# Kernel tuning notes

Measured on AMD Instinct MI355X. Metric: run time of the kernel, lower is better.

## Reference

```python
import jax, jax.numpy as jnp
import numpy as np

H = 512   # lstm_hidden_size
B = 64    # batch
S = 256   # seqlen


def setup_inputs() -> dict:
    key = jax.random.key(0)
    ks = jax.random.split(key, 6)
    scale = 1.0 / np.sqrt(H)  # PyTorch LSTM default init range
    return {
        "x": jax.random.normal(ks[0], (B, S, 2 * H), dtype=jnp.float32),
        "hi": jax.random.normal(ks[1], (B, S, 2 * H), dtype=jnp.float32),
        "W_ih": jax.random.uniform(ks[2], (4 * H, 5 * H), minval=-scale, maxval=scale, dtype=jnp.float32),
        "W_hh": jax.random.uniform(ks[3], (4 * H, H), minval=-scale, maxval=scale, dtype=jnp.float32),
        "b_ih": jax.random.uniform(ks[4], (4 * H,), minval=-scale, maxval=scale, dtype=jnp.float32),
        "b_hh": jax.random.uniform(ks[5], (4 * H,), minval=-scale, maxval=scale, dtype=jnp.float32),
    }


def _forward(x, hi, W_ih, W_hh, b_ih, b_hh):
    h_dim = W_hh.shape[1]
    bias = b_ih + b_hh
    xc = jnp.concatenate([x, hi], axis=-1)          # [B, S, 4H]
    xc = jnp.transpose(xc, (1, 0, 2))               # [S, B, 4H]
    batch = xc.shape[1]

    def cell(hc, inp_b):
        # inp_b: [5H]; PyTorch LSTM treats the batch dim as seq (batch_first=False quirk)
        h, c = hc
        gates = inp_b @ W_ih.T + h @ W_hh.T + bias  # [4H]
        i_g, f_g, g_g, o_g = jnp.split(gates, 4)
        i_g = jax.nn.sigmoid(i_g)
        f_g = jax.nn.sigmoid(f_g)
        g_g = jnp.tanh(g_g)
        o_g = jax.nn.sigmoid(o_g)
        c = f_g * c + i_g * g_g
        h = o_g * jnp.tanh(c)
        return (h, c), h

    def step(carry, x_i):
        out_prev, h, c = carry                      # out_prev: [B, H]
        inp = jnp.concatenate([x_i, out_prev], axis=-1)  # [B, 5H]
        (h, c), outs = jax.lax.scan(cell, (h, c), inp)    # scan over batch dim
        return (outs, h, c), outs

    init = (jnp.zeros((batch, h_dim), x.dtype),
            jnp.zeros((h_dim,), x.dtype),
            jnp.zeros((h_dim,), x.dtype))
    _, all_out = jax.lax.scan(step, init, xc)       # [S, B, H]
    return jnp.transpose(all_out, (1, 0, 2))        # [B, S, H]


def reference(x, hi, W_ih, W_hh, b_ih, b_hh):
    # Dropout layers are identity in eval mode.
    return _forward(x, hi, W_ih, W_hh, b_ih, b_hh)
```

## Files before the change

kernel.cpp:

```cpp
#include <hip/hip_runtime.h>

typedef _Float16 f16;
typedef _Float16 f16x2 __attribute__((ext_vector_type(2)));
typedef _Float16 f16x4 __attribute__((ext_vector_type(4)));
typedef _Float16 f16x8 __attribute__((ext_vector_type(8)));
typedef float f32x4 __attribute__((ext_vector_type(4)));
typedef unsigned int u32;
typedef unsigned int u32x4 __attribute__((ext_vector_type(4)));
typedef unsigned long long ull;

#define HD 512
#define T_TOT 16384
#define RING 128
#define NWG 32
#define NTH 512

static const size_t O_XC    = 0;
static const size_t O_W1    = 67108864;
static const size_t O_WHH   = 75497472;
static const size_t O_W2    = 77594624;
static const size_t O_G     = 79691776;
static const size_t O_PRING = 213909504;

__device__ __forceinline__ float dot2f(f16x2 a, f16x2 b, float c) {
#if __has_builtin(__builtin_amdgcn_fdot2)
    return __builtin_amdgcn_fdot2(a, b, c, false);
#else
    return fmaf((float)a[0], (float)b[0], fmaf((float)a[1], (float)b[1], c));
#endif
}
__device__ __forceinline__ f16x2 bcf(u32 u) { return __builtin_bit_cast(f16x2, u); }

__device__ __forceinline__ float sigf(float x) { return 1.0f / (1.0f + __expf(-x)); }
__device__ __forceinline__ float tanhfast(float x) { return 1.0f - 2.0f / (__expf(2.0f * x) + 1.0f); }

__device__ __forceinline__ ull ld_a64(const ull* p) {
    return __hip_atomic_load(p, __ATOMIC_RELAXED, __HIP_MEMORY_SCOPE_AGENT);
}
__device__ __forceinline__ void st_a64(ull* p, ull v) {
    __hip_atomic_store(p, v, __ATOMIC_RELAXED, __HIP_MEMORY_SCOPE_AGENT);
}

__global__ __launch_bounds__(256) void conv_xc(const float* __restrict__ x,
                                               const float* __restrict__ hi,
                                               f16* __restrict__ xc) {
    int gid = blockIdx.x * 256 + threadIdx.x;
    int t = gid >> 9;
    int k = (gid & 511) << 2;
    int b = t & 63, s = t >> 6;
    const float* src = (k < 1024) ? (x  + ((size_t)((b << 8) + s) << 10) + k)
                                  : (hi + ((size_t)((b << 8) + s) << 10) + (k - 1024));
    float4 v = *reinterpret_cast<const float4*>(src);
    f16x4 o = { (_Float16)v.x, (_Float16)v.y, (_Float16)v.z, (_Float16)v.w };
    *reinterpret_cast<f16x4*>(xc + ((size_t)t << 11) + k) = o;
}

__global__ __launch_bounds__(256) void conv_w1(const float* __restrict__ wih,
                                               f16* __restrict__ w1) {
    int gid = blockIdx.x * 256 + threadIdx.x;
    int j = gid >> 9;
    int k = (gid & 511) << 2;
    float4 v = *reinterpret_cast<const float4*>(wih + (size_t)j * 2560 + k);
    f16x4 o = { (_Float16)v.x, (_Float16)v.y, (_Float16)v.z, (_Float16)v.w };
    *reinterpret_cast<f16x4*>(w1 + ((size_t)j << 11) + k) = o;
}

__global__ __launch_bounds__(256) void conv_wc(const float* __restrict__ whh,
                                               const float* __restrict__ wih,
                                               f16* __restrict__ whhf,
                                               f16* __restrict__ w2f) {
    int gid = blockIdx.x * 256 + threadIdx.x;
    int j = gid >> 7;
    int k = (gid & 127) << 2;
    float4 a = *reinterpret_cast<const float4*>(whh + (size_t)j * 512 + k);
    f16x4 oa = { (_Float16)a.x, (_Float16)a.y, (_Float16)a.z, (_Float16)a.w };
    *reinterpret_cast<f16x4*>(whhf + ((size_t)j << 9) + k) = oa;
    float4 bv = *reinterpret_cast<const float4*>(wih + (size_t)j * 2560 + 2048 + k);
    f16x4 ob = { (_Float16)bv.x, (_Float16)bv.y, (_Float16)bv.z, (_Float16)bv.w };
    *reinterpret_cast<f16x4*>(w2f + ((size_t)j << 9) + k) = ob;
}

__global__ __launch_bounds__(256) void gemm_pre(const f16* __restrict__ XC,
                                                const f16* __restrict__ W1,
                                                const float* __restrict__ b_ih,
                                                const float* __restrict__ b_hh,
                                                float* __restrict__ G) {
    int w = threadIdx.x >> 6, l = threadIdx.x & 63;
    int R0 = blockIdx.y * 128 + (w >> 1) * 64;
    int C0 = blockIdx.x * 128 + (w & 1) * 64;
    int lr = l & 15, kb = l >> 4;
    f32x4 acc[4][4] = {};
    const f16* Abase = XC + (size_t)(R0 + lr) * 2048 + kb * 8;
    const f16* Bbase = W1 + (size_t)(C0 + lr) * 2048 + kb * 8;
    for (int kk = 0; kk < 2048; kk += 32) {
        f16x8 av[4], bv[4];
#pragma unroll
        for (int i = 0; i < 4; i++)
            av[i] = *reinterpret_cast<const f16x8*>(Abase + (size_t)(i * 16) * 2048 + kk);
#pragma unroll
        for (int i = 0; i < 4; i++)
            bv[i] = *reinterpret_cast<const f16x8*>(Bbase + (size_t)(i * 16) * 2048 + kk);
#pragma unroll
        for (int fr = 0; fr < 4; fr++)
#pragma unroll
            for (int fc = 0; fc < 4; fc++)
                acc[fr][fc] = __builtin_amdgcn_mfma_f32_16x16x32_f16(av[fr], bv[fc], acc[fr][fc], 0, 0, 0);
    }
#pragma unroll
    for (int fc = 0; fc < 4; fc++) {
        int col = C0 + fc * 16 + lr;
        float bias = b_ih[col] + b_hh[col];
#pragma unroll
        for (int fr = 0; fr < 4; fr++) {
#pragma unroll
            for (int r = 0; r < 4; r++) {
                int row = R0 + fr * 16 + kb * 4 + r;
                G[(size_t)row * 2048 + col] = acc[fr][fc][r] + bias;
            }
        }
    }
}

__global__ __launch_bounds__(NTH, 1) void lstm_chain(const float* __restrict__ G,
                                                     const f16* __restrict__ Whhf,
                                                     const f16* __restrict__ W2f,
                                                     ull* __restrict__ ring,
                                                     float* __restrict__ out) {
    const int wg = blockIdx.x;
    const int tid = threadIdx.x;
    const int wv = tid >> 6, l = tid & 63;
    const int g = wv & 3, uh = wv >> 2;
    const int rr = ((l & 1) << 2) | (l & 2) | ((l >> 2) & 1);
    const int row0 = g * 512 + wg * 16 + uh * 8;
    const int growD = row0 + rr;

    __shared__ u32 hist[64][256];
    __shared__ __align__(16) float part[2][16][4];

    for (int i = tid; i < 4096; i += NTH)
        reinterpret_cast<u32x4*>(hist)[i] = (u32x4){0u, 0u, 0u, 0u};

    u32 wu1[32], wu2[32];
#pragma unroll
    for (int r = 0; r < 8; r++) {
        u32x4 a = __builtin_bit_cast(u32x4,
            *reinterpret_cast<const f16x8*>(Whhf + (size_t)(row0 + r) * 512 + 8 * l));
        u32x4 b = __builtin_bit_cast(u32x4,
            *reinterpret_cast<const f16x8*>(W2f + (size_t)(row0 + r) * 512 + 8 * l));
        wu1[r * 4 + 0] = a.x; wu1[r * 4 + 1] = a.y; wu1[r * 4 + 2] = a.z; wu1[r * 4 + 3] = a.w;
        wu2[r * 4 + 0] = b.x; wu2[r * 4 + 1] = b.y; wu2[r * 4 + 2] = b.z; wu2[r * 4 + 3] = b.w;
    }
#pragma unroll
    for (int i = 0; i < 32; i++)
        asm volatile("" : "+v"(wu1[i]), "+v"(wu2[i]));

    float cst = 0.0f;
    float gv = (l < 8) ? G[growD] : 0.0f;
    __syncthreads();

    for (int t = 0; t < T_TOT; t++) {
        const int buf = t & 1;

        u32x4 hv = *reinterpret_cast<const u32x4*>(&hist[t & 63][4 * l]);
        float ac[8] = {0.f, 0.f, 0.f, 0.f, 0.f, 0.f, 0.f, 0.f};
        {
            f16x2 h0 = bcf(hv.x), h1 = bcf(hv.y), h2 = bcf(hv.z), h3 = bcf(hv.w);
#pragma unroll
            for (int r = 0; r < 8; r++) {
                ac[r] = dot2f(bcf(wu2[r * 4 + 0]), h0, ac[r]);
                ac[r] = dot2f(bcf(wu2[r * 4 + 1]), h1, ac[r]);
                ac[r] = dot2f(bcf(wu2[r * 4 + 2]), h2, ac[r]);
                ac[r] = dot2f(bcf(wu2[r * 4 + 3]), h3, ac[r]);
            }
        }

        const ull* pB = ring + (size_t)((t - 1) & (RING - 1)) * 256 + 4 * l;
        const u32 want = (u32)t;
        ull b0 = ld_a64(pB + 0), b1 = ld_a64(pB + 1);
        ull b2 = ld_a64(pB + 2), b3 = ld_a64(pB + 3);
        while ((((u32)(b0 >> 32) ^ want) | ((u32)(b1 >> 32) ^ want) |
                ((u32)(b2 >> 32) ^ want) | ((u32)(b3 >> 32) ^ want)) != 0u) {
            b0 = ld_a64(pB + 0); b1 = ld_a64(pB + 1);
            b2 = ld_a64(pB + 2); b3 = ld_a64(pB + 3);
        }

        int tn = (t + 1 < T_TOT) ? t + 1 : t;
        float gnext = (l < 8) ? G[(size_t)tn * 2048 + growD] : 0.0f;

        if (wv == 0)
            *reinterpret_cast<u32x4*>(&hist[(t - 1) & 63][4 * l]) =
                (u32x4){(u32)b0, (u32)b1, (u32)b2, (u32)b3};

        {
            f16x2 h0 = bcf((u32)b0), h1 = bcf((u32)b1), h2 = bcf((u32)b2), h3 = bcf((u32)b3);
#pragma unroll
            for (int r = 0; r < 8; r++) {
                ac[r] = dot2f(bcf(wu1[r * 4 + 0]), h0, ac[r]);
                ac[r] = dot2f(bcf(wu1[r * 4 + 1]), h1, ac[r]);
                ac[r] = dot2f(bcf(wu1[r * 4 + 2]), h2, ac[r]);
                ac[r] = dot2f(bcf(wu1[r * 4 + 3]), h3, ac[r]);
            }
        }

        const bool s0 = l & 1, s1 = l & 2, s2 = l & 4;
        float b4_0 = (s0 ? ac[4] : ac[0]) + __shfl_xor((s0 ? ac[0] : ac[4]), 1);
        float b4_1 = (s0 ? ac[5] : ac[1]) + __shfl_xor((s0 ? ac[1] : ac[5]), 1);
        float b4_2 = (s0 ? ac[6] : ac[2]) + __shfl_xor((s0 ? ac[2] : ac[6]), 1);
        float b4_3 = (s0 ? ac[7] : ac[3]) + __shfl_xor((s0 ? ac[3] : ac[7]), 1);
        float c2_0 = (s1 ? b4_2 : b4_0) + __shfl_xor((s1 ? b4_0 : b4_2), 2);
        float c2_1 = (s1 ? b4_3 : b4_1) + __shfl_xor((s1 ? b4_1 : b4_3), 2);
        float d    = (s2 ? c2_1 : c2_0) + __shfl_xor((s2 ? c2_0 : c2_1), 4);
        d += __shfl_xor(d, 8);
        d += __shfl_xor(d, 16);
        d += __shfl_xor(d, 32);
        if (l < 8)
            part[buf][uh * 8 + rr][g] = d + gv;
        gv = gnext;
        __syncthreads();

        const int u = l & 15;
        float4 pg = *reinterpret_cast<const float4*>(part[buf][u]);
        float fi = sigf(pg.x), ff = sigf(pg.y);
        float fgg = tanhfast(pg.z), fo = sigf(pg.w);
        cst = ff * cst + fi * fgg;
        float h = fo * tanhfast(cst);

        u32 hb = (u32)__builtin_bit_cast(unsigned short, (f16)h);
        u32 plo = (u32)__shfl((int)hb, 2 * (l & 7));
        u32 phi = (u32)__shfl((int)hb, 2 * (l & 7) + 1);
        ull pv = (ull)(plo & 0xffffu) | ((ull)(phi & 0xffffu) << 16) |
                 ((ull)(u32)(t + 1) << 32);
        if (wv == 0 && l < 8)
            st_a64(ring + (size_t)(t & (RING - 1)) * 256 + wg * 8 + l, pv);
        if (wv == 1 && l < 16) {
            int b = t & 63, s = t >> 6;
            out[((size_t)((b << 8) + s)) * 512 + wg * 16 + l] = h;
        }
    }
}

extern "C" void kernel_launch(void* const* d_in, const int* in_sizes, int n_in,
                              void* d_out, int out_size, void* d_ws, size_t ws_size,
                              hipStream_t stream) {
    const float* x    = (const float*)d_in[0];
    const float* hi   = (const float*)d_in[1];
    const float* W_ih = (const float*)d_in[2];
    const float* W_hh = (const float*)d_in[3];
    const float* b_ih = (const float*)d_in[4];
    const float* b_hh = (const float*)d_in[5];

    char* ws = (char*)d_ws;
    f16*   XCf   = (f16*)(ws + O_XC);
    f16*   W1f   = (f16*)(ws + O_W1);
    f16*   Whhf  = (f16*)(ws + O_WHH);
    f16*   W2f   = (f16*)(ws + O_W2);
    float* G     = (float*)(ws + O_G);
    ull*   ring  = (ull*)(ws + O_PRING);

    hipMemsetAsync(ring, 0, (size_t)RING * 256 * sizeof(ull), stream);

    conv_xc<<<32768, 256, 0, stream>>>(x, hi, XCf);
    conv_w1<<<4096, 256, 0, stream>>>(W_ih, W1f);
    conv_wc<<<1024, 256, 0, stream>>>(W_hh, W_ih, Whhf, W2f);
    gemm_pre<<<dim3(16, 128), 256, 0, stream>>>(XCf, W1f, b_ih, b_hh, G);
    lstm_chain<<<NWG, NTH, 0, stream>>>(G, Whhf, W2f, ring, (float*)d_out);
}
```

Measured before the change: 30.51 ms.

## Restructure LSTM chain to 64 single-wave blocks without LDS or barriers

The recurrent chain kernel moves from 32 workgroups of 8 waves to 64 single-wave workgroups. Each wave holds 32 rows of both recurrent weight matrices in registers, loaded with inline-asm vector loads. The intra-block shared-memory partial-sum exchange and __syncthreads per step are replaced by a wider shuffle reduction. The local LDS history buffer is dropped and the delayed h is reread from the global ring (slot t+64). This removes per-step barrier and LDS latency from the serial critical path, at the cost of very high register pressure per lane, more global ring traffic, and double the number of inter-block flag polls.

```diff
diff --git a/kernel.cpp b/kernel.cpp
--- a/kernel.cpp
+++ b/kernel.cpp
@@ -12,8 +12,7 @@
 #define HD 512
 #define T_TOT 16384
 #define RING 128
-#define NWG 32
-#define NTH 512
+#define NWAVE 64
 
 static const size_t O_XC    = 0;
 static const size_t O_W1    = 67108864;
@@ -121,60 +120,86 @@
     }
 }
 
-__global__ __launch_bounds__(NTH, 1) void lstm_chain(const float* __restrict__ G,
-                                                     const f16* __restrict__ Whhf,
-                                                     const f16* __restrict__ W2f,
-                                                     ull* __restrict__ ring,
-                                                     float* __restrict__ out) {
-    const int wg = blockIdx.x;
-    const int tid = threadIdx.x;
-    const int wv = tid >> 6, l = tid & 63;
-    const int g = wv & 3, uh = wv >> 2;
-    const int rr = ((l & 1) << 2) | (l & 2) | ((l >> 2) & 1);
-    const int row0 = g * 512 + wg * 16 + uh * 8;
-    const int growD = row0 + rr;
-
-    __shared__ u32 hist[64][256];
-    __shared__ __align__(16) float part[2][16][4];
-
-    for (int i = tid; i < 4096; i += NTH)
-        reinterpret_cast<u32x4*>(hist)[i] = (u32x4){0u, 0u, 0u, 0u};
-
-    u32 wu1[32], wu2[32];
-#pragma unroll
-    for (int r = 0; r < 8; r++) {
-        u32x4 a = __builtin_bit_cast(u32x4,
-            *reinterpret_cast<const f16x8*>(Whhf + (size_t)(row0 + r) * 512 + 8 * l));
-        u32x4 b = __builtin_bit_cast(u32x4,
-            *reinterpret_cast<const f16x8*>(W2f + (size_t)(row0 + r) * 512 + 8 * l));
-        wu1[r * 4 + 0] = a.x; wu1[r * 4 + 1] = a.y; wu1[r * 4 + 2] = a.z; wu1[r * 4 + 3] = a.w;
-        wu2[r * 4 + 0] = b.x; wu2[r * 4 + 1] = b.y; wu2[r * 4 + 2] = b.z; wu2[r * 4 + 3] = b.w;
-    }
-#pragma unroll
-    for (int i = 0; i < 32; i++)
-        asm volatile("" : "+v"(wu1[i]), "+v"(wu2[i]));
+#define WLOAD16(OUT, P0, P1, P2, P3)                                        \
+    asm volatile(                                                            \
+        "global_load_dwordx4 %0, %16, off\n\t"                               \
+        "global_load_dwordx4 %1, %16, off offset:1024\n\t"                   \
+        "global_load_dwordx4 %2, %16, off offset:2048\n\t"                   \
+        "global_load_dwordx4 %3, %16, off offset:3072\n\t"                   \
+        "global_load_dwordx4 %4, %17, off\n\t"                               \
+        "global_load_dwordx4 %5, %17, off offset:1024\n\t"                   \
+        "global_load_dwordx4 %6, %17, off offset:2048\n\t"                   \
+        "global_load_dwordx4 %7, %17, off offset:3072\n\t"                   \
+        "global_load_dwordx4 %8, %18, off\n\t"                               \
+        "global_load_dwordx4 %9, %18, off offset:1024\n\t"                   \
+        "global_load_dwordx4 %10, %18, off offset:2048\n\t"                  \
+        "global_load_dwordx4 %11, %18, off offset:3072\n\t"                  \
+        "global_load_dwordx4 %12, %19, off\n\t"                              \
+        "global_load_dwordx4 %13, %19, off offset:1024\n\t"                  \
+        "global_load_dwordx4 %14, %19, off offset:2048\n\t"                  \
+        "global_load_dwordx4 %15, %19, off offset:3072\n\t"                  \
+        "s_waitcnt vmcnt(0)"                                                 \
+        : "=&v"(OUT[0]), "=&v"(OUT[1]), "=&v"(OUT[2]), "=&v"(OUT[3]),        \
+          "=&v"(OUT[4]), "=&v"(OUT[5]), "=&v"(OUT[6]), "=&v"(OUT[7]),        \
+          "=&v"(OUT[8]), "=&v"(OUT[9]), "=&v"(OUT[10]), "=&v"(OUT[11]),      \
+          "=&v"(OUT[12]), "=&v"(OUT[13]), "=&v"(OUT[14]), "=&v"(OUT[15])     \
+        : "v"(P0), "v"(P1), "v"(P2), "v"(P3) : "memory")
+
+__global__ __launch_bounds__(64, 1) void lstm_chain(const float* __restrict__ G,
+                                                    const f16* __restrict__ Whhf,
+                                                    const f16* __restrict__ W2f,
+                                                    ull* __restrict__ ring,
+                                                    float* __restrict__ out) {
+    const int w = blockIdx.x;
+    const int l = threadIdx.x;
+
+    u32x4 w1v[32], w2v[32];
+    {
+        const f16* base1 = Whhf + (size_t)(8 * w) * 512 + 8 * l;
+        const f16* base2 = W2f + (size_t)(8 * w) * 512 + 8 * l;
+        const size_t gstride = (size_t)512 * 512;
+        WLOAD16((&w1v[0]),  base1,               base1 + 4 * 512,
+                            base1 + gstride,     base1 + gstride + 4 * 512);
+        WLOAD16((&w1v[16]), base1 + 2 * gstride, base1 + 2 * gstride + 4 * 512,
+                            base1 + 3 * gstride, base1 + 3 * gstride + 4 * 512);
+        WLOAD16((&w2v[0]),  base2,               base2 + 4 * 512,
+                            base2 + gstride,     base2 + gstride + 4 * 512);
+        WLOAD16((&w2v[16]), base2 + 2 * gstride, base2 + 2 * gstride + 4 * 512,
+                            base2 + 3 * gstride, base2 + 3 * gstride + 4 * 512);
+    }
+
+    const int lm = l & 31;
+    const int rIdx = ((lm & 1) << 4) | ((lm & 2) << 2) | (lm & 4) |
+                     ((lm & 8) >> 2) | ((lm & 16) >> 4);
+    const size_t grow = (size_t)(rIdx >> 3) * 512 + 8 * w + (rIdx & 7);
+    const int ub = ((l & 1) << 4) | ((l & 2) << 2) | (l & 4);
 
     float cst = 0.0f;
-    float gv = (l < 8) ? G[growD] : 0.0f;
-    __syncthreads();
+    float gcur = G[grow];
 
     for (int t = 0; t < T_TOT; t++) {
-        const int buf = t & 1;
-
-        u32x4 hv = *reinterpret_cast<const u32x4*>(&hist[t & 63][4 * l]);
-        float ac[8] = {0.f, 0.f, 0.f, 0.f, 0.f, 0.f, 0.f, 0.f};
+        const int slotA = (t + 64) & (RING - 1);
+        const int slotB = (t - 1) & (RING - 1);
+
+        float ac[32];
+#pragma unroll
+        for (int r = 0; r < 32; r++) ac[r] = 0.0f;
+
         {
-            f16x2 h0 = bcf(hv.x), h1 = bcf(hv.y), h2 = bcf(hv.z), h3 = bcf(hv.w);
-#pragma unroll
-            for (int r = 0; r < 8; r++) {
-                ac[r] = dot2f(bcf(wu2[r * 4 + 0]), h0, ac[r]);
-                ac[r] = dot2f(bcf(wu2[r * 4 + 1]), h1, ac[r]);
-                ac[r] = dot2f(bcf(wu2[r * 4 + 2]), h2, ac[r]);
-                ac[r] = dot2f(bcf(wu2[r * 4 + 3]), h3, ac[r]);
+            const ull* pA = ring + (size_t)slotA * 256 + 4 * l;
+            ull a0 = ld_a64(pA + 0), a1 = ld_a64(pA + 1);
+            ull a2 = ld_a64(pA + 2), a3 = ld_a64(pA + 3);
+            f16x2 h0 = bcf((u32)a0), h1 = bcf((u32)a1), h2 = bcf((u32)a2), h3 = bcf((u32)a3);
+#pragma unroll
+            for (int r = 0; r < 32; r++) {
+                ac[r] = dot2f(bcf(w2v[r].x), h0, ac[r]);
+                ac[r] = dot2f(bcf(w2v[r].y), h1, ac[r]);
+                ac[r] = dot2f(bcf(w2v[r].z), h2, ac[r]);
+                ac[r] = dot2f(bcf(w2v[r].w), h3, ac[r]);
             }
         }
 
-        const ull* pB = ring + (size_t)((t - 1) & (RING - 1)) * 256 + 4 * l;
+        const ull* pB = ring + (size_t)slotB * 256 + 4 * l;
         const u32 want = (u32)t;
         ull b0 = ld_a64(pB + 0), b1 = ld_a64(pB + 1);
         ull b2 = ld_a64(pB + 2), b3 = ld_a64(pB + 3);
@@ -185,56 +210,60 @@
         }
 
         int tn = (t + 1 < T_TOT) ? t + 1 : t;
-        float gnext = (l < 8) ? G[(size_t)tn * 2048 + growD] : 0.0f;
-
-        if (wv == 0)
-            *reinterpret_cast<u32x4*>(&hist[(t - 1) & 63][4 * l]) =
-                (u32x4){(u32)b0, (u32)b1, (u32)b2, (u32)b3};
+        float gnext = G[(size_t)tn * 2048 + grow];
 
         {
             f16x2 h0 = bcf((u32)b0), h1 = bcf((u32)b1), h2 = bcf((u32)b2), h3 = bcf((u32)b3);
 #pragma unroll
-            for (int r = 0; r < 8; r++) {
-                ac[r] = dot2f(bcf(wu1[r * 4 + 0]), h0, ac[r]);
-                ac[r] = dot2f(bcf(wu1[r * 4 + 1]), h1, ac[r]);
-                ac[r] = dot2f(bcf(wu1[r * 4 + 2]), h2, ac[r]);
-                ac[r] = dot2f(bcf(wu1[r * 4 + 3]), h3, ac[r]);
+            for (int r = 0; r < 32; r++) {
+                ac[r] = dot2f(bcf(w1v[r].x), h0, ac[r]);
+                ac[r] = dot2f(bcf(w1v[r].y), h1, ac[r]);
+                ac[r] = dot2f(bcf(w1v[r].z), h2, ac[r]);
+                ac[r] = dot2f(bcf(w1v[r].w), h3, ac[r]);
             }
         }
 
-        const bool s0 = l & 1, s1 = l & 2, s2 = l & 4;
-        float b4_0 = (s0 ? ac[4] : ac[0]) + __shfl_xor((s0 ? ac[0] : ac[4]), 1);
-        float b4_1 = (s0 ? ac[5] : ac[1]) + __shfl_xor((s0 ? ac[1] : ac[5]), 1);
-        float b4_2 = (s0 ? ac[6] : ac[2]) + __shfl_xor((s0 ? ac[2] : ac[6]), 1);
-        float b4_3 = (s0 ? ac[7] : ac[3]) + __shfl_xor((s0 ? ac[3] : ac[7]), 1);
-        float c2_0 = (s1 ? b4_2 : b4_0) + __shfl_xor((s1 ? b4_0 : b4_2), 2);
-        float c2_1 = (s1 ? b4_3 : b4_1) + __shfl_xor((s1 ? b4_1 : b4_3), 2);
-        float d    = (s2 ? c2_1 : c2_0) + __shfl_xor((s2 ? c2_0 : c2_1), 4);
-        d += __shfl_xor(d, 8);
-        d += __shfl_xor(d, 16);
+        const bool s0 = l & 1, s1 = l & 2, s2 = l & 4, s3 = l & 8, s4 = l & 16;
+        float v16[16];
+#pragma unroll
+        for (int r = 0; r < 16; r++)
+            v16[r] = (s0 ? ac[r + 16] : ac[r]) + __shfl_xor((s0 ? ac[r] : ac[r + 16]), 1);
+        float v8[8];
+#pragma unroll
+        for (int r = 0; r < 8; r++)
+            v8[r] = (s1 ? v16[r + 8] : v16[r]) + __shfl_xor((s1 ? v16[r] : v16[r + 8]), 2);
+        float v4[4];
+#pragma unroll
+        for (int r = 0; r < 4; r++)
+            v4[r] = (s2 ? v8[r + 4] : v8[r]) + __shfl_xor((s2 ? v8[r] : v8[r + 4]), 4);
+        float v2[2];
+#pragma unroll
+        for (int r = 0; r < 2; r++)
+            v2[r] = (s3 ? v4[r + 2] : v4[r]) + __shfl_xor((s3 ? v4[r] : v4[r + 2]), 8);
+        float d = (s4 ? v2[1] : v2[0]) + __shfl_xor((s4 ? v2[0] : v2[1]), 16);
         d += __shfl_xor(d, 32);
-        if (l < 8)
-            part[buf][uh * 8 + rr][g] = d + gv;
-        gv = gnext;
-        __syncthreads();
-
-        const int u = l & 15;
-        float4 pg = *reinterpret_cast<const float4*>(part[buf][u]);
-        float fi = sigf(pg.x), ff = sigf(pg.y);
-        float fgg = tanhfast(pg.z), fo = sigf(pg.w);
+
+        d += gcur;
+        gcur = gnext;
+
+        float vi = __shfl(d, ub);
+        float vf = __shfl(d, ub | 2);
+        float vg = __shfl(d, ub | 1);
+        float vo = __shfl(d, ub | 3);
+        float fi = sigf(vi), ff = sigf(vf), fgg = tanhfast(vg), fo = sigf(vo);
         cst = ff * cst + fi * fgg;
         float h = fo * tanhfast(cst);
 
         u32 hb = (u32)__builtin_bit_cast(unsigned short, (f16)h);
-        u32 plo = (u32)__shfl((int)hb, 2 * (l & 7));
-        u32 phi = (u32)__shfl((int)hb, 2 * (l & 7) + 1);
+        u32 plo = (u32)__shfl((int)hb, 2 * (l & 3));
+        u32 phi = (u32)__shfl((int)hb, 2 * (l & 3) + 1);
         ull pv = (ull)(plo & 0xffffu) | ((ull)(phi & 0xffffu) << 16) |
                  ((ull)(u32)(t + 1) << 32);
-        if (wv == 0 && l < 8)
-            st_a64(ring + (size_t)(t & (RING - 1)) * 256 + wg * 8 + l, pv);
-        if (wv == 1 && l < 16) {
+        if (l < 4)
+            st_a64(ring + (size_t)(t & (RING - 1)) * 256 + w * 4 + l, pv);
+        if (l < 8) {
             int b = t & 63, s = t >> 6;
-            out[((size_t)((b << 8) + s)) * 512 + wg * 16 + l] = h;
+            out[((size_t)((b << 8) + s)) * 512 + w * 8 + l] = h;
         }
     }
 }
@@ -263,5 +292,5 @@
     conv_w1<<<4096, 256, 0, stream>>>(W_ih, W1f);
     conv_wc<<<1024, 256, 0, stream>>>(W_hh, W_ih, Whhf, W2f);
     gemm_pre<<<dim3(16, 128), 256, 0, stream>>>(XCf, W1f, b_ih, b_hh, G);
-    lstm_chain<<<NWG, NTH, 0, stream>>>(G, Whhf, W2f, ring, (float*)d_out);
-}
+    lstm_chain<<<NWAVE, 64, 0, stream>>>(G, Whhf, W2f, ring, (float*)d_out);
+}
```

After: 48.12 ms. +57.7%, slower.
